# Kernel tuning notes

Measured on AMD Instinct MI355X. Metric: run time of the kernel, lower is better.

The kernel has to match this reference:

```python
import jax, jax.numpy as jnp
import numpy as np

N, F, FP, K = 4096, 512, 64, 8
ALPHA = 0.2  # leaky relu slope
NEG_INF = -1e16


def setup_inputs() -> dict:
    key = jax.random.key(0)
    k1, k2, k3, k4 = jax.random.split(key, 4)
    gain = np.sqrt(2.0 / (1.0 + ALPHA ** 2))
    node_matrix = jax.random.normal(k1, (N, F), dtype=jnp.float32)
    adjacency_matrix = jax.random.randint(k2, (N, N), 0, 2, dtype=jnp.int32)
    W = jax.random.normal(k3, (K, F, FP), dtype=jnp.float32) * (gain * np.sqrt(2.0 / (F + FP)))
    a = jax.random.normal(k4, (K, 2 * FP, 1), dtype=jnp.float32) * (gain * np.sqrt(2.0 / (2 * FP + 1)))
    return {"node_matrix": node_matrix, "adjacency_matrix": adjacency_matrix, "W": W, "a": a}


def reference(node_matrix, adjacency_matrix, W, a):
    # hidden_repr: [K, N, F']
    h = jnp.einsum('nf,kfp->knp', node_matrix, W)
    a_src = a[:, :FP, 0]   # applied to attended-to node j (first half -> row vector)
    a_dst = a[:, FP:, 0]   # applied to query node i (second half -> column vector)
    f1 = jnp.einsum('knp,kp->kn', h, a_src)  # [K, N] scores for j
    f2 = jnp.einsum('knp,kp->kn', h, a_dst)  # [K, N] scores for i
    # e[k, i, j] = LeakyReLU(f2[k, i] + f1[k, j])  -> [K, N, N]
    e = jax.nn.leaky_relu(f2[:, :, None] + f1[:, None, :], negative_slope=ALPHA)
    e = jnp.where(adjacency_matrix[None, :, :] > 0, e, NEG_INF)
    att = jax.nn.softmax(e, axis=-1)
    out = jnp.einsum('knm,kmp->knp', att, h)  # [K, N, F']
    # concat heads along feature dim -> [N, K*F']
    return jnp.transpose(out, (1, 0, 2)).reshape(N, K * FP)
```

## Files before the change

kernel.cpp:

```cpp
#include <hip/hip_runtime.h>

#define N 4096
#define F 512
#define FP 64
#define K 8
#define KFP 512
#define LOG2E 1.44269504088896f

#define BI 64
#define BJ 256
#define NTILE (N / BJ)

typedef __attribute__((ext_vector_type(8))) short short8;
typedef __attribute__((ext_vector_type(4))) float f32x4;

__device__ __forceinline__ unsigned short f2bs(float x) {
  union { __bf16 b; unsigned short u; } u;
  u.b = (__bf16)x;
  return u.u;
}

#if __has_builtin(__builtin_amdgcn_exp2f)
#define EXP2(x) __builtin_amdgcn_exp2f(x)
#else
#define EXP2(x) __expf((x) * 0.6931471805599453f)
#endif

__device__ __forceinline__ int sext_bit(unsigned v, int off) {
#if __has_builtin(__builtin_amdgcn_sbfe)
  return __builtin_amdgcn_sbfe((int)v, off, 1);
#else
  return ((int)(v << (31 - off))) >> 31;
#endif
}

__device__ __forceinline__ float mask_w(float w, unsigned mb, int off) {
  return __int_as_float(__float_as_int(w) & sext_bit(mb, off));
}

__global__ __launch_bounds__(256) void prep_fused(const float* __restrict__ X,
                                                  unsigned short* __restrict__ Xb,
                                                  const float* __restrict__ W,
                                                  unsigned short* __restrict__ Wt) {
  __shared__ unsigned short WT16[64][66];
  const int t = threadIdx.x;
  if (blockIdx.x < 1024) {
    const int idx = (blockIdx.x * 256 + t) * 8;
    const float4 v0 = *reinterpret_cast<const float4*>(&X[idx]);
    const float4 v1 = *reinterpret_cast<const float4*>(&X[idx + 4]);
    unsigned short o[8] = {f2bs(v0.x), f2bs(v0.y), f2bs(v0.z), f2bs(v0.w),
                           f2bs(v1.x), f2bs(v1.y), f2bs(v1.z), f2bs(v1.w)};
    *reinterpret_cast<uint4*>(&Xb[idx]) = *reinterpret_cast<uint4*>(&o[0]);
    return;
  }
  const int bid = blockIdx.x - 1024;
  const int k = bid >> 3;
  const int f0 = (bid & 7) * 64;
#pragma unroll
  for (int j = 0; j < 16; j++) {
    const int idx = j * 256 + t;
    const int fl = idx >> 6, p = idx & 63;
    WT16[p][fl] = f2bs(W[(k * F + f0 + fl) * FP + p]);
  }
  __syncthreads();
  const int p = t >> 2, uc = t & 3;
  unsigned short tmp[16];
#pragma unroll
  for (int j = 0; j < 16; j++) tmp[j] = WT16[p][uc * 16 + j];
  unsigned short* dst = &Wt[(k * 64 + p) * F + f0 + uc * 16];
  *reinterpret_cast<uint4*>(dst)     = *reinterpret_cast<uint4*>(&tmp[0]);
  *reinterpret_cast<uint4*>(dst + 8) = *reinterpret_cast<uint4*>(&tmp[8]);
}

__global__ __launch_bounds__(256, 2) void gemm_h(
    const unsigned short* __restrict__ Xb, const unsigned short* __restrict__ Wt,
    const float* __restrict__ a, unsigned short* __restrict__ h_bT,
    float* __restrict__ f1, float* __restrict__ f2,
    const int* __restrict__ adj, unsigned long long* __restrict__ adjb) {
  __shared__ __align__(16) unsigned char AT[2][8192];
  __shared__ __align__(16) unsigned char BT[2][8192];
  __shared__ float F1L[2][64], F2L[2][64];

  const int t = threadIdx.x;
  const int k = blockIdx.x & 7;
  const int n0 = (blockIdx.x >> 3) * 64;
  const int wave = t >> 6, lane = t & 63;
  const int cg = wave >> 1, ng = wave & 1;
  const int col = lane & 15, kg = lane >> 4;
  const unsigned short* __restrict__ Wk = Wt + (size_t)k * 64 * F;

  f32x4 acc[2][2];
#pragma unroll
  for (int i = 0; i < 2; i++)
#pragma unroll
    for (int j = 0; j < 2; j++) acc[i][j] = (f32x4){0.f, 0.f, 0.f, 0.f};

  auto stage = [&](int tt, int buf) {
    const int f0 = tt * 64;
#pragma unroll
    for (int m = 0; m < 2; m++) {
      const int g = wave * 128 + m * 64 + lane;
      const int row = g >> 3, pu = g & 7;
      const int u = pu ^ (row & 7);
      const void* srcA = Wk + (size_t)row * F + f0 + u * 8;
      void* dstA = (void*)(AT[buf] + (wave * 128 + m * 64) * 16);
      __builtin_amdgcn_global_load_lds(
          (const __attribute__((address_space(1))) void*)srcA,
          (__attribute__((address_space(3))) void*)dstA, 16, 0, 0);
      const void* srcB = Xb + (size_t)(n0 + row) * F + f0 + u * 8;
      void* dstB = (void*)(BT[buf] + (wave * 128 + m * 64) * 16);
      __builtin_amdgcn_global_load_lds(
          (const __attribute__((address_space(1))) void*)srcB,
          (__attribute__((address_space(3))) void*)dstB, 16, 0, 0);
    }
  };

  auto compute = [&](int buf) {
#pragma unroll
    for (int ks = 0; ks < 2; ks++) {
      const int u0 = ks * 4 + kg;
      short8 af[2], bf[2];
#pragma unroll
      for (int i = 0; i < 2; i++) {
        const int rowA = cg * 32 + i * 16 + col;
        af[i] = *reinterpret_cast<const short8*>(
            AT[buf] + (rowA * 8 + (u0 ^ (rowA & 7))) * 16);
        const int rowB = ng * 32 + i * 16 + col;
        bf[i] = *reinterpret_cast<const short8*>(
            BT[buf] + (rowB * 8 + (u0 ^ (rowB & 7))) * 16);
      }
#pragma unroll
      for (int i = 0; i < 2; i++)
#pragma unroll
        for (int j = 0; j < 2; j++)
          acc[i][j] = __builtin_amdgcn_mfma_f32_16x16x32_bf16(af[i], bf[j], acc[i][j], 0, 0, 0);
    }
  };

  int adjv[16];
  const int wb_wave = blockIdx.x * 512 + wave * 128;
  auto adj_load = [&](int c) {
    const int* p = adj + (size_t)(wb_wave + c * 16) * 64 + lane;
#pragma unroll
    for (int x = 0; x < 16; x++) adjv[x] = p[x * 64];
  };
  auto adj_process = [&](int c) {
    unsigned long long ms[16];
#pragma unroll
    for (int x = 0; x < 16; x++) ms[x] = __ballot(adjv[x] > 0);
    if (lane == 0) {
#pragma unroll
      for (int x = 0; x < 16; x++) adjb[wb_wave + c * 16 + x] = ms[x];
    }
  };

  stage(0, 0);
  adj_load(0);
  for (int tt = 0; tt < F / 64; ++tt) {
    const int cur = tt & 1;
    __builtin_amdgcn_s_barrier();
    __builtin_amdgcn_sched_barrier(0);
    if (tt + 1 < F / 64) {
      stage(tt + 1, 1 - cur);
      asm volatile("s_waitcnt vmcnt(4)" ::: "memory");
    } else {
      asm volatile("s_waitcnt vmcnt(0)" ::: "memory");
    }
    __builtin_amdgcn_s_barrier();
    __builtin_amdgcn_sched_barrier(0);
    if (tt >= 1) {
      adj_process(tt - 1);
      adj_load(tt);
    }
    compute(cur);
  }
  asm volatile("s_waitcnt vmcnt(0)" ::: "memory");
  adj_process(7);

  float p1[2] = {0.f, 0.f}, p2[2] = {0.f, 0.f};
#pragma unroll
  for (int i = 0; i < 2; i++) {
#pragma unroll
    for (int r = 0; r < 4; r++) {
      const int p = cg * 32 + i * 16 + kg * 4 + r;
      const float as = a[k * 128 + p];
      const float ad = a[k * 128 + 64 + p];
#pragma unroll
      for (int j = 0; j < 2; j++) {
        const float v = acc[i][j][r];
        h_bT[(size_t)(k * 64 + p) * N + n0 + ng * 32 + j * 16 + col] = f2bs(v);
        p1[j] = fmaf(v, as, p1[j]);
        p2[j] = fmaf(v, ad, p2[j]);
      }
    }
  }
#pragma unroll
  for (int j = 0; j < 2; j++) {
    p1[j] += __shfl_xor(p1[j], 16); p1[j] += __shfl_xor(p1[j], 32);
    p2[j] += __shfl_xor(p2[j], 16); p2[j] += __shfl_xor(p2[j], 32);
    if (kg == 0) {
      F1L[cg][ng * 32 + j * 16 + col] = p1[j];
      F2L[cg][ng * 32 + j * 16 + col] = p2[j];
    }
  }
  __syncthreads();
  if (t < 64) {
    f1[k * N + n0 + t] = (F1L[0][t] + F1L[1][t]) * LOG2E;
    f2[k * N + n0 + t] = (F2L[0][t] + F2L[1][t]) * LOG2E;
  }
}

__global__ __launch_bounds__(512, 4) void attn_mfma(
    const unsigned short* __restrict__ h_bT, const float* __restrict__ f1,
    const float* __restrict__ f2, const unsigned long long* __restrict__ adjb,
    float* __restrict__ out) {
  __shared__ __align__(16) unsigned char SMEM[65536];
  __shared__ float DL[2][4][32];

  const int tid = threadIdx.x;
  const int k = blockIdx.x & 7;
  const int i0 = (blockIdx.x >> 3) * BI;
  const int wave = tid >> 6, lane = tid & 63;
  const int iq = wave >> 2;
  const int jq = wave & 3;
  const int col = lane & 15, kg = lane >> 4;

  const float* __restrict__ f1k = f1 + k * N;
  const unsigned char* __restrict__ hbb =
      (const unsigned char*)(h_bT + (size_t)k * 64 * N);

  const int rbase = i0 + iq * 32;
  const float f2r0 = f2[k * N + rbase + col];
  const float f2r1 = f2[k * N + rbase + 16 + col];
  const unsigned long long* __restrict__ arow0 = adjb + (size_t)(rbase + col) * 64;
  const unsigned long long* __restrict__ arow1 = adjb + (size_t)(rbase + 16 + col) * 64;

  f32x4 acc[2][4];
  f32x4 accden[2];
#pragma unroll
  for (int a = 0; a < 2; a++) {
    accden[a] = (f32x4){0.f, 0.f, 0.f, 0.f};
#pragma unroll
    for (int n = 0; n < 4; n++) acc[a][n] = (f32x4){0.f, 0.f, 0.f, 0.f};
  }
  short8 bones;
#pragma unroll
  for (int e = 0; e < 8; e++) bones[e] = (short)0x3F80;

  auto stage = [&](int tt, int buf) {
#pragma unroll
    for (int m = 0; m < 4; m++) {
      const int g = wave * 4 + m;
      const int row = g * 2 + (lane >> 5);
      const int pu = lane & 31;
      const int u = pu ^ (row & 15);
      const void* src = hbb + (size_t)row * (N * 2) + tt * (BJ * 2) + u * 16;
      void* dst = (void*)(SMEM + buf * 32768 + g * 1024);
      __builtin_amdgcn_global_load_lds(
          (const __attribute__((address_space(1))) void*)src,
          (__attribute__((address_space(3))) void*)dst, 16, 0, 0);
    }
  };

  auto compute_tile = [&](int tt, int buf) {
    const uint2 aw0 = *reinterpret_cast<const uint2*>(arow0 + tt * 4 + jq);
    const uint2 aw1 = *reinterpret_cast<const uint2*>(arow1 + tt * 4 + jq);
#pragma unroll
    for (int ks = 0; ks < 2; ks++) {
      const int jglob = tt * BJ + jq * 64 + ks * 32;
      const float4 fa = *reinterpret_cast<const float4*>(&f1k[jglob + kg * 8]);
      const float4 fb = *reinterpret_cast<const float4*>(&f1k[jglob + kg * 8 + 4]);

      short8 bfrag[4];
#pragma unroll
      for (int n = 0; n < 4; n++) {
        const int row_b = n * 16 + col;
        const int u = jq * 8 + ks * 4 + kg;
        const int pu = u ^ col;
        bfrag[n] = *reinterpret_cast<const short8*>(
            SMEM + buf * 32768 + row_b * 512 + pu * 16);
      }

      const unsigned mb0 = (ks ? aw0.y : aw0.x) >> (kg * 8);
      const unsigned mb1 = (ks ? aw1.y : aw1.x) >> (kg * 8);
      const float fv[8] = {fa.x, fa.y, fa.z, fa.w, fb.x, fb.y, fb.z, fb.w};

      union { unsigned u[4]; short8 s; } A0, A1;
#pragma unroll
      for (int e2 = 0; e2 < 4; e2++) {
        const float va = fv[2 * e2], vb = fv[2 * e2 + 1];
        float t0a = f2r0 + va, t0b = f2r0 + vb;
        float t1a = f2r1 + va, t1b = f2r1 + vb;
        t0a = fmaxf(t0a, 0.2f * t0a); t0b = fmaxf(t0b, 0.2f * t0b);
        t1a = fmaxf(t1a, 0.2f * t1a); t1b = fmaxf(t1b, 0.2f * t1b);
        float w0a = EXP2(t0a), w0b = EXP2(t0b);
        float w1a = EXP2(t1a), w1b = EXP2(t1b);
        w0a = mask_w(w0a, mb0, 2 * e2); w0b = mask_w(w0b, mb0, 2 * e2 + 1);
        w1a = mask_w(w1a, mb1, 2 * e2); w1b = mask_w(w1b, mb1, 2 * e2 + 1);
        asm("v_cvt_pk_bf16_f32 %0, %1, %2" : "=v"(A0.u[e2]) : "v"(w0a), "v"(w0b));
        asm("v_cvt_pk_bf16_f32 %0, %1, %2" : "=v"(A1.u[e2]) : "v"(w1a), "v"(w1b));
      }

      accden[0] = __builtin_amdgcn_mfma_f32_16x16x32_bf16(A0.s, bones, accden[0], 0, 0, 0);
      accden[1] = __builtin_amdgcn_mfma_f32_16x16x32_bf16(A1.s, bones, accden[1], 0, 0, 0);
#pragma unroll
      for (int n = 0; n < 4; n++) {
        acc[0][n] = __builtin_amdgcn_mfma_f32_16x16x32_bf16(A0.s, bfrag[n], acc[0][n], 0, 0, 0);
        acc[1][n] = __builtin_amdgcn_mfma_f32_16x16x32_bf16(A1.s, bfrag[n], acc[1][n], 0, 0, 0);
      }
    }
  };

  stage(0, 0);
  for (int t = 0; t < NTILE; ++t) {
    const int cur = t & 1;
    __builtin_amdgcn_s_barrier();
    __builtin_amdgcn_sched_barrier(0);
    if (t + 1 < NTILE) {
      stage(t + 1, 1 - cur);
      asm volatile("s_waitcnt vmcnt(4)" ::: "memory");
    } else {
      asm volatile("s_waitcnt vmcnt(0)" ::: "memory");
    }
    __builtin_amdgcn_s_barrier();
    __builtin_amdgcn_sched_barrier(0);
    compute_tile(t, cur);
  }
  __syncthreads();

  float* CL = (float*)SMEM;
  if (jq != 0) {
#pragma unroll
    for (int a = 0; a < 2; a++) {
#pragma unroll
      for (int n = 0; n < 4; n++)
#pragma unroll
        for (int r = 0; r < 4; r++)
          CL[((iq * 3 + (jq - 1)) * 32 + a * 16 + kg * 4 + r) * 66 + n * 16 + col] =
              acc[a][n][r];
      if (col == 0)
#pragma unroll
        for (int r = 0; r < 4; r++) DL[iq][jq][a * 16 + kg * 4 + r] = accden[a][r];
    }
  } else {
#pragma unroll
    for (int a = 0; a < 2; a++)
      if (col == 0)
#pragma unroll
        for (int r = 0; r < 4; r++) DL[iq][0][a * 16 + kg * 4 + r] = accden[a][r];
  }
  __syncthreads();
  if (jq == 0) {
#pragma unroll
    for (int a = 0; a < 2; a++) {
#pragma unroll
      for (int r = 0; r < 4; r++) {
        const int il = a * 16 + kg * 4 + r;
        const float den = DL[iq][0][il] + DL[iq][1][il] + DL[iq][2][il] + DL[iq][3][il];
        const float rinv = 1.f / den;
#pragma unroll
        for (int n = 0; n < 4; n++) {
          float v = acc[a][n][r];
          v += CL[((iq * 3 + 0) * 32 + il) * 66 + n * 16 + col];
          v += CL[((iq * 3 + 1) * 32 + il) * 66 + n * 16 + col];
          v += CL[((iq * 3 + 2) * 32 + il) * 66 + n * 16 + col];
          out[(size_t)(i0 + iq * 32 + il) * KFP + k * 64 + n * 16 + col] = v * rinv;
        }
      }
    }
  }
}

extern "C" void kernel_launch(void* const* d_in, const int* in_sizes, int n_in,
                              void* d_out, int out_size, void* d_ws, size_t ws_size,
                              hipStream_t stream) {
  const float* X   = (const float*)d_in[0];
  const int*   adj = (const int*)d_in[1];
  const float* W   = (const float*)d_in[2];
  const float* a   = (const float*)d_in[3];
  float* out = (float*)d_out;

  char* ws = (char*)d_ws;
  unsigned short* h_bT = (unsigned short*)(ws);
  float* f1  = (float*)(ws + 4194304);
  float* f2  = (float*)(ws + 4325376);
  unsigned long long* adjb = (unsigned long long*)(ws + 4456448);
  unsigned short* Wt = (unsigned short*)(ws + 6553600);
  unsigned short* Xb = (unsigned short*)d_out;

  hipLaunchKernelGGL(prep_fused, dim3(1024 + K * (F / 64)), dim3(256), 0, stream,
                     X, Xb, W, Wt);
  hipLaunchKernelGGL(gemm_h, dim3(K * (N / 64)), dim3(256), 0, stream,
                     Xb, Wt, a, h_bT, f1, f2, adj, adjb);
  hipLaunchKernelGGL(attn_mfma, dim3((N / BI) * K), dim3(512), 0, stream,
                     h_bT, f1, f2, adjb, out);
}
```

Baseline: 85.97 us.

## Prefetch f1 and adjacency bits a tile ahead, use packed fp32 math

The per-tile f1 score vectors and adjacency mask words are now loaded one tile ahead into registers, interleaved with the LDS staging, and the vmcnt waits are retuned for the larger number of loads in flight. This hides global-load latency that previously sat right before the exp/mask work. The LeakyReLU add and multiply use v_pk_add_f32/v_pk_mul_f32 to cut VALU instruction count. The MFMA block is wrapped in s_setprio to favour matrix issue. In exchange, register pressure rises from the prefetch buffers, and the hand-written waitcnt counts must stay in step with the load order.

```diff
diff --git a/kernel.cpp b/kernel.cpp
--- a/kernel.cpp
+++ b/kernel.cpp
@@ -13,6 +13,7 @@
 
 typedef __attribute__((ext_vector_type(8))) short short8;
 typedef __attribute__((ext_vector_type(4))) float f32x4;
+typedef __attribute__((ext_vector_type(2))) float f32x2;
 
 __device__ __forceinline__ unsigned short f2bs(float x) {
   union { __bf16 b; unsigned short u; } u;
@@ -26,16 +27,19 @@
 #define EXP2(x) __expf((x) * 0.6931471805599453f)
 #endif
 
-__device__ __forceinline__ int sext_bit(unsigned v, int off) {
-#if __has_builtin(__builtin_amdgcn_sbfe)
-  return __builtin_amdgcn_sbfe((int)v, off, 1);
-#else
-  return ((int)(v << (31 - off))) >> 31;
-#endif
+__device__ __forceinline__ f32x2 pk_add(f32x2 a, f32x2 b) {
+  f32x2 d;
+  asm("v_pk_add_f32 %0, %1, %2" : "=v"(d) : "v"(a), "v"(b));
+  return d;
+}
+__device__ __forceinline__ f32x2 pk_mul(f32x2 a, f32x2 b) {
+  f32x2 d;
+  asm("v_pk_mul_f32 %0, %1, %2" : "=v"(d) : "v"(a), "v"(b));
+  return d;
 }
 
 __device__ __forceinline__ float mask_w(float w, unsigned mb, int off) {
-  return __int_as_float(__float_as_int(w) & sext_bit(mb, off));
+  return __int_as_float(__float_as_int(w) & __builtin_amdgcn_sbfe((int)mb, off, 1));
 }
 
 __global__ __launch_bounds__(256) void prep_fused(const float* __restrict__ X,
@@ -232,6 +236,9 @@
   const int rbase = i0 + iq * 32;
   const float f2r0 = f2[k * N + rbase + col];
   const float f2r1 = f2[k * N + rbase + 16 + col];
+  const f32x2 f2r0_2 = {f2r0, f2r0};
+  const f32x2 f2r1_2 = {f2r1, f2r1};
+  const f32x2 c02 = {0.2f, 0.2f};
   const unsigned long long* __restrict__ arow0 = adjb + (size_t)(rbase + col) * 64;
   const unsigned long long* __restrict__ arow1 = adjb + (size_t)(rbase + 16 + col) * 64;
 
@@ -262,14 +269,26 @@
     }
   };
 
-  auto compute_tile = [&](int tt, int buf) {
-    const uint2 aw0 = *reinterpret_cast<const uint2*>(arow0 + tt * 4 + jq);
-    const uint2 aw1 = *reinterpret_cast<const uint2*>(arow1 + tt * 4 + jq);
+  float4 pf[4];
+  uint2 pw[2];
+  auto pload = [&](int tt) {
+    const int jb = tt * BJ + jq * 64 + kg * 8;
+    pf[0] = *reinterpret_cast<const float4*>(&f1k[jb]);
+    pf[1] = *reinterpret_cast<const float4*>(&f1k[jb + 4]);
+    pf[2] = *reinterpret_cast<const float4*>(&f1k[jb + 32]);
+    pf[3] = *reinterpret_cast<const float4*>(&f1k[jb + 36]);
+    pw[0] = *reinterpret_cast<const uint2*>(arow0 + tt * 4 + jq);
+    pw[1] = *reinterpret_cast<const uint2*>(arow1 + tt * 4 + jq);
+  };
+
+  auto compute_tile = [&](int buf, float4 fA0, float4 fB0, float4 fA1, float4 fB1,
+                          uint2 aw0, uint2 aw1) {
 #pragma unroll
     for (int ks = 0; ks < 2; ks++) {
-      const int jglob = tt * BJ + jq * 64 + ks * 32;
-      const float4 fa = *reinterpret_cast<const float4*>(&f1k[jglob + kg * 8]);
-      const float4 fb = *reinterpret_cast<const float4*>(&f1k[jglob + kg * 8 + 4]);
+      const float4 fa = ks ? fA1 : fA0;
+      const float4 fb = ks ? fB1 : fB0;
+      const unsigned m0 = ks ? aw0.y : aw0.x;
+      const unsigned m1 = ks ? aw1.y : aw1.x;
 
       short8 bfrag[4];
 #pragma unroll
@@ -281,26 +300,26 @@
             SMEM + buf * 32768 + row_b * 512 + pu * 16);
       }
 
-      const unsigned mb0 = (ks ? aw0.y : aw0.x) >> (kg * 8);
-      const unsigned mb1 = (ks ? aw1.y : aw1.x) >> (kg * 8);
-      const float fv[8] = {fa.x, fa.y, fa.z, fa.w, fb.x, fb.y, fb.z, fb.w};
-
+      const f32x2 prs[4] = {{fa.x, fa.y}, {fa.z, fa.w}, {fb.x, fb.y}, {fb.z, fb.w}};
       union { unsigned u[4]; short8 s; } A0, A1;
 #pragma unroll
       for (int e2 = 0; e2 < 4; e2++) {
-        const float va = fv[2 * e2], vb = fv[2 * e2 + 1];
-        float t0a = f2r0 + va, t0b = f2r0 + vb;
-        float t1a = f2r1 + va, t1b = f2r1 + vb;
-        t0a = fmaxf(t0a, 0.2f * t0a); t0b = fmaxf(t0b, 0.2f * t0b);
-        t1a = fmaxf(t1a, 0.2f * t1a); t1b = fmaxf(t1b, 0.2f * t1b);
-        float w0a = EXP2(t0a), w0b = EXP2(t0b);
-        float w1a = EXP2(t1a), w1b = EXP2(t1b);
-        w0a = mask_w(w0a, mb0, 2 * e2); w0b = mask_w(w0b, mb0, 2 * e2 + 1);
-        w1a = mask_w(w1a, mb1, 2 * e2); w1b = mask_w(w1b, mb1, 2 * e2 + 1);
+        const f32x2 t0 = pk_add(prs[e2], f2r0_2);
+        const f32x2 t1 = pk_add(prs[e2], f2r1_2);
+        const f32x2 u0 = pk_mul(t0, c02);
+        const f32x2 u1 = pk_mul(t1, c02);
+        float w0a = EXP2(fmaxf(t0.x, u0.x));
+        float w0b = EXP2(fmaxf(t0.y, u0.y));
+        float w1a = EXP2(fmaxf(t1.x, u1.x));
+        float w1b = EXP2(fmaxf(t1.y, u1.y));
+        const int ob = kg * 8 + 2 * e2;
+        w0a = mask_w(w0a, m0, ob);     w0b = mask_w(w0b, m0, ob + 1);
+        w1a = mask_w(w1a, m1, ob);     w1b = mask_w(w1b, m1, ob + 1);
         asm("v_cvt_pk_bf16_f32 %0, %1, %2" : "=v"(A0.u[e2]) : "v"(w0a), "v"(w0b));
         asm("v_cvt_pk_bf16_f32 %0, %1, %2" : "=v"(A1.u[e2]) : "v"(w1a), "v"(w1b));
       }
 
+      __builtin_amdgcn_s_setprio(1);
       accden[0] = __builtin_amdgcn_mfma_f32_16x16x32_bf16(A0.s, bones, accden[0], 0, 0, 0);
       accden[1] = __builtin_amdgcn_mfma_f32_16x16x32_bf16(A1.s, bones, accden[1], 0, 0, 0);
 #pragma unroll
@@ -308,23 +327,28 @@
         acc[0][n] = __builtin_amdgcn_mfma_f32_16x16x32_bf16(A0.s, bfrag[n], acc[0][n], 0, 0, 0);
         acc[1][n] = __builtin_amdgcn_mfma_f32_16x16x32_bf16(A1.s, bfrag[n], acc[1][n], 0, 0, 0);
       }
+      __builtin_amdgcn_s_setprio(0);
     }
   };
 
   stage(0, 0);
+  pload(0);
   for (int t = 0; t < NTILE; ++t) {
     const int cur = t & 1;
     __builtin_amdgcn_s_barrier();
     __builtin_amdgcn_sched_barrier(0);
     if (t + 1 < NTILE) {
       stage(t + 1, 1 - cur);
-      asm volatile("s_waitcnt vmcnt(4)" ::: "memory");
+      asm volatile("s_waitcnt vmcnt(10)" ::: "memory");
     } else {
-      asm volatile("s_waitcnt vmcnt(0)" ::: "memory");
+      asm volatile("s_waitcnt vmcnt(6)" ::: "memory");
     }
     __builtin_amdgcn_s_barrier();
     __builtin_amdgcn_sched_barrier(0);
-    compute_tile(t, cur);
+    const float4 cf0 = pf[0], cf1 = pf[1], cf2 = pf[2], cf3 = pf[3];
+    const uint2 cw0 = pw[0], cw1 = pw[1];
+    if (t + 1 < NTILE) pload(t + 1);
+    compute_tile(cur, cf0, cf1, cf2, cf3, cw0, cw1);
   }
   __syncthreads();
 
```

New measurement: 113.4 us. 31.9% more time.
